# Kernel tuning notes

Hardware: AMD Instinct MI355X
Metric: run time of the kernel (lower is better)

## Reference

```python
import jax, jax.numpy as jnp
import numpy as np

CEP_ORDER = 24
ALPHA = 0.42
BETA = 0.2
ONSET = 2
IR_LENGTH = 128


def _freqt_matrix(in_order, out_order, alpha):
    # diffsptk FrequencyTransform precomputed matrix A (L2, L1): c2 = c1 @ A.T
    L1, L2 = in_order + 1, out_order + 1
    A = np.zeros((L2, L1), dtype=np.float64)
    A[0, :] = alpha ** np.arange(L1)
    if L2 > 1 and L1 > 1:
        A[1, 1:] = (alpha ** np.arange(L1 - 1, dtype=np.float64)) * np.arange(1, L1) * (1.0 - alpha * alpha)
    for i in range(2, L2):
        for j in range(1, L1):
            A[i, j] = A[i - 1, j - 1] + alpha * (A[i, j - 1] - A[i - 1, j])
    return A


def _mc2b_matrix(M, alpha):
    # b[m] = mc[m] - alpha*b[m+1]  =>  b[m] = sum_{j>=m} (-alpha)^(j-m) mc[j]
    j = np.arange(M + 1)
    P = j[None, :] - j[:, None]
    return np.where(P >= 0, (-alpha) ** np.maximum(P, 0), 0.0)


def _b2mc_matrix(M, alpha):
    # mc[m] = b[m] + alpha*b[m+1]
    return np.eye(M + 1) + alpha * np.eye(M + 1, k=1)


# constants derived from hyperparameters (buffers in the torch module)
A_FT = jnp.asarray(_freqt_matrix(CEP_ORDER, IR_LENGTH - 1, -ALPHA), dtype=jnp.float32)   # (128, 25)
A_MC2B = jnp.asarray(_mc2b_matrix(CEP_ORDER, ALPHA), dtype=jnp.float32)                  # (25, 25)
A_B2MC = jnp.asarray(_b2mc_matrix(CEP_ORDER, ALPHA), dtype=jnp.float32)                  # (25, 25)
_w = np.full(CEP_ORDER + 1, 1.0 + BETA, dtype=np.float32)
_w[:ONSET] = 1.0
WEIGHT = jnp.asarray(_w)                                                                  # (25,)


def _mc2en(mc):
    # mel-cepstrum -> energy: warp to linear cepstrum (len 128), power spectrum, r[0]
    c = jnp.einsum('...m,lm->...l', mc, A_FT)                 # (..., 128)
    spec = jnp.exp(2.0 * jnp.fft.rfft(c, n=IR_LENGTH).real)   # (..., 65), real power spectrum
    # r[0] of irfft(spec): DC + Nyquist once, interior bins twice (IR_LENGTH even)
    r0 = (spec[..., 0] + spec[..., -1] + 2.0 * jnp.sum(spec[..., 1:-1], axis=-1)) / IR_LENGTH
    return r0                                                  # (...,)


def setup_inputs() -> dict:
    key = jax.random.key(0)
    mc = 0.2 * jax.random.normal(key, (16, 32768, CEP_ORDER + 1), dtype=jnp.float32)
    return {"mc": mc}


def reference(mc):
    e1 = _mc2en(mc)                                            # energy before postfilter
    mc2 = mc * WEIGHT                                          # intensity-weighted cepstrum
    e2 = _mc2en(mc2)                                           # energy after weighting
    b2 = jnp.einsum('...m,nm->...n', mc2, A_MC2B)              # mc -> MLSA coefficients
    b2 = b2.at[..., 0].add(0.5 * jnp.log(e1 / e2))             # energy compensation on b[0]
    return jnp.einsum('...m,nm->...n', b2, A_B2MC)             # MLSA -> mel-cepstrum
```

## Files before the change

### kernel.cpp

```cpp
#include <hip/hip_runtime.h>


namespace cg {

constexpr int L  = 128;
constexpr int M1 = 25;

struct CosTab { double v[L]; };
constexpr CosTab make_costab() {
    CosTab t{};
    const double PI = 3.14159265358979323846;
    for (int i = 0; i < L; ++i) {
        int j = (i <= 64) ? i : i - 128;
        double x = (2.0 * PI * (double)j) / 128.0;
        double x2 = x * x, term = 1.0, s = 1.0;
        for (int n = 1; n <= 16; ++n) {
            term *= -x2 / ((2.0 * n - 1.0) * (2.0 * n));
            s += term;
        }
        t.v[i] = s;
    }
    return t;
}
constexpr CosTab CT = make_costab();

struct AMat { double v[L][M1]; };
constexpr AMat make_aft() {
    AMat A{};
    const double al = -0.42;
    double p = 1.0;
    for (int j = 0; j < M1; ++j) { A.v[0][j] = p; p *= al; }
    double q = 1.0;
    for (int j = 1; j < M1; ++j) { A.v[1][j] = q * (double)j * (1.0 - al * al); q *= al; }
    for (int i = 2; i < L; ++i)
        for (int j = 1; j < M1; ++j)
            A.v[i][j] = A.v[i - 1][j - 1] + al * (A.v[i][j - 1] - A.v[i - 1][j]);
    return A;
}
constexpr AMat AFT = make_aft();

struct Chunk { double v[8][M1]; };
template <int K0>
constexpr Chunk make_chunk() {
    Chunk c{};
    for (int kk = 0; kk < 8; ++kk) {
        int k = K0 + kk;
        for (int m = 0; m < M1; ++m) {
            double s = 0.0;
            for (int l = 0; l < L; ++l)
                s += AFT.v[l][m] * CT.v[(k * l) & 127];
            c.v[kk][m] = s;
        }
    }
    return c;
}
constexpr Chunk CH0 = make_chunk<0>();
constexpr Chunk CH1 = make_chunk<8>();
constexpr Chunk CH2 = make_chunk<16>();
constexpr Chunk CH3 = make_chunk<24>();
constexpr Chunk CH4 = make_chunk<32>();
constexpr Chunk CH5 = make_chunk<40>();
constexpr Chunk CH6 = make_chunk<48>();
constexpr Chunk CH7 = make_chunk<56>();
constexpr Chunk CH8 = make_chunk<64>();

constexpr double chunkval(int bin, int m) {
    const Chunk* chs[9] = { &CH0, &CH1, &CH2, &CH3, &CH4, &CH5, &CH6, &CH7, &CH8 };
    return chs[bin >> 3]->v[bin & 7][m];
}

constexpr double blogical(int k, int col) {
    const double LOG2E = 1.44269504088896340736;
    if (col >= 130) return (k == 25) ? -1.0e4 : 0.0;
    int bin = (col < 65) ? col : (col - 65);
    if (k == 25) return (bin == 0 || bin == 64) ? 0.0 : 1.0;
    if (k > 25) return 0.0;
    double c = LOG2E * 2.0 * chunkval(bin, k);
    if (col >= 65 && k >= 2) c *= 1.2;
    return c;
}

constexpr unsigned short f2h(double v) {
    if (v == 0.0) return 0;
    unsigned short s = 0;
    if (v < 0) { s = 0x8000; v = -v; }
    int e = 0;
    while (v >= 2.0) { v *= 0.5; ++e; }
    while (v < 1.0)  { v *= 2.0; --e; }
    if (e > 15) return (unsigned short)(s | 0x7c00);
    if (e < -14) return s;
    int mant = (int)((v - 1.0) * 1024.0 + 0.5);
    if (mant == 1024) { mant = 0; ++e; if (e > 15) return (unsigned short)(s | 0x7c00); }
    return (unsigned short)(s | ((e + 15) << 10) | mant);
}

struct Tile { unsigned short v[64][8]; };
template <int N>
constexpr Tile make_tile() {
    Tile t{};
    for (int l = 0; l < 64; ++l)
        for (int j = 0; j < 8; ++j)
            t.v[l][j] = f2h(blogical((l >> 4) * 8 + j, N * 16 + (l & 15)));
    return t;
}
constexpr Tile T0 = make_tile<0>();
constexpr Tile T1 = make_tile<1>();
constexpr Tile T2 = make_tile<2>();
constexpr Tile T3 = make_tile<3>();
constexpr Tile T4 = make_tile<4>();
constexpr Tile T5 = make_tile<5>();
constexpr Tile T6 = make_tile<6>();
constexpr Tile T7 = make_tile<7>();
constexpr Tile T8 = make_tile<8>();

struct BH { alignas(16) unsigned short v[9][64][8]; };
constexpr BH make_bh() {
    BH b{};
    const Tile* ts[9] = { &T0, &T1, &T2, &T3, &T4, &T5, &T6, &T7, &T8 };
    for (int n = 0; n < 9; ++n)
        for (int l = 0; l < 64; ++l)
            for (int j = 0; j < 8; ++j)
                b.v[n][l][j] = ts[n]->v[l][j];
    return b;
}

}

__device__ const cg::BH g_Bh = cg::make_bh();

typedef _Float16 f16x8 __attribute__((ext_vector_type(8)));
typedef float    f32x4 __attribute__((ext_vector_type(4)));

constexpr int WCHUNK = 1672;

__global__ __launch_bounds__(256, 6)
void mcpf_kernel(const float* __restrict__ mc, float* __restrict__ out) {
    __shared__ __align__(16) float sbuf[4 * WCHUNK];
    const int tid  = threadIdx.x;
    const int lane = tid & 63;
    const int wv   = tid >> 6;
    const int r0   = lane & 15;
    const int kg   = lane >> 4;

    float* __restrict__ wbuf = &sbuf[wv * WCHUNK];
    float* __restrict__ dreg = wbuf + 1600;

    const long long base4 = (long long)blockIdx.x * 1600 + wv * 400;

    f16x8 bfrag[9];
#pragma unroll
    for (int n = 0; n < 9; ++n)
        bfrag[n] = *reinterpret_cast<const f16x8*>(&g_Bh.v[n][lane][0]);

    const float4* __restrict__ src4 =
        reinterpret_cast<const float4*>(mc) + base4;
    float4* wb4 = reinterpret_cast<float4*>(wbuf);
#pragma unroll
    for (int j = 0; j < 7; ++j) {
        int idx = lane + j * 64;
        if (idx < 400) wb4[idx] = src4[idx];
    }
    asm volatile("s_waitcnt lgkmcnt(0)" ::: "memory");

#pragma unroll
    for (int g = 0; g < 4; ++g) {
        const int rowbase = g * 16;
        const float* __restrict__ arow = &wbuf[(rowbase + r0) * 25 + kg * 8];

        float tmp[8];
#pragma unroll
        for (int j = 0; j < 8; ++j) tmp[j] = arow[j];
        f16x8 af;
        af[0] = (_Float16)tmp[0];
        af[1] = (kg == 3) ? (_Float16)1.0f : (_Float16)tmp[1];
#pragma unroll
        for (int j = 2; j < 8; ++j)
            af[j] = (kg == 3) ? (_Float16)0.0f : (_Float16)tmp[j];

        float s1 = 0.0f, s2 = 0.0f;
#pragma unroll
        for (int n = 0; n < 9; ++n) {
            f32x4 acc = {0.f, 0.f, 0.f, 0.f};
            acc = __builtin_amdgcn_mfma_f32_16x16x32_f16(bfrag[n], af, acc, 0, 0, 0);
            float e0 = __builtin_amdgcn_exp2f(acc[0]);
            float e1 = __builtin_amdgcn_exp2f(acc[1]);
            float e2 = __builtin_amdgcn_exp2f(acc[2]);
            float e3 = __builtin_amdgcn_exp2f(acc[3]);
            if (n < 4) {
                s1 += (e0 + e1) + (e2 + e3);
            } else if (n == 4) {
                float h = (e0 + e1) + (e2 + e3);
                bool c = (kg == 0);
                s1 += c ? e0 : 0.0f;
                s2 += c ? (h - e0) : h;
            } else {
                s2 += (e0 + e1) + (e2 + e3);
            }
        }

        s1 += __shfl_xor(s1, 16);
        s1 += __shfl_xor(s1, 32);
        s2 += __shfl_xor(s2, 16);
        s2 += __shfl_xor(s2, 32);

        if (kg == 0) {
            float d = 0.34657359027997264f *
                      (__builtin_amdgcn_logf(s1) - __builtin_amdgcn_logf(s2));
            dreg[rowbase + r0] = d;
        }
    }

    asm volatile("s_waitcnt lgkmcnt(0)" ::: "memory");

    float4* __restrict__ dst4 = reinterpret_cast<float4*>(out) + base4;
#pragma unroll
    for (int j = 0; j < 7; ++j) {
        int idx = lane + j * 64;
        if (idx < 400) {
            float4 v = wb4[idx];
            int f = idx * 4;
            int q = f / 25;
            int r = f - 25 * q;
            float dv0 = dreg[q];
            float dv1 = dreg[q + 1];
            v.x *= (r     < 2)                  ? 1.0f : 1.2f;
            v.y *= (r + 1 < 2 || r + 1 == 25)   ? 1.0f : 1.2f;
            v.z *= (r + 2 == 25 || r + 2 == 26) ? 1.0f : 1.2f;
            v.w *= (r + 3 == 25 || r + 3 == 26) ? 1.0f : 1.2f;
            if (r == 0)  v.x += dv0;
            if (r == 22) v.w += dv1;
            if (r == 23) v.z += dv1;
            if (r == 24) v.y += dv1;
            dst4[idx] = v;
        }
    }
}

extern "C" void kernel_launch(void* const* d_in, const int* in_sizes, int n_in,
                              void* d_out, int out_size, void* d_ws, size_t ws_size,
                              hipStream_t stream) {
    const float* mc = (const float*)d_in[0];
    float* out = (float*)d_out;
    const int rows = in_sizes[0] / 25;
    const int blocks = rows / 256;
    mcpf_kernel<<<dim3(blocks), dim3(256), 0, stream>>>(mc, out);
}
```

Measured before the change: 24.54 us.

## Load rows directly from global into registers, dropping LDS staging

Removes the shared-memory staging buffer. Each lane now loads its 8-float slice of a row straight from global memory with unaligned 4-float vector loads and writes the scaled output back from registers, adding the energy correction inline. This cuts LDS traffic, the per-element div/mod index math and the waits, and lowers the occupancy hint from 6 to 4. Global accesses now use 100-byte row strides, so coalescing is worse, and loads issued as dword4 with only 4-byte alignment may be split.

After: 64.34 us. 162% more time.

```diff
diff --git a/kernel.cpp b/kernel.cpp
--- a/kernel.cpp
+++ b/kernel.cpp
@@ -130,52 +130,50 @@
 
 typedef _Float16 f16x8 __attribute__((ext_vector_type(8)));
 typedef float    f32x4 __attribute__((ext_vector_type(4)));
-
-constexpr int WCHUNK = 1672;
-
-__global__ __launch_bounds__(256, 6)
+typedef float    f32x4a4 __attribute__((ext_vector_type(4), aligned(4)));
+
+__global__ __launch_bounds__(256, 4)
 void mcpf_kernel(const float* __restrict__ mc, float* __restrict__ out) {
-    __shared__ __align__(16) float sbuf[4 * WCHUNK];
     const int tid  = threadIdx.x;
     const int lane = tid & 63;
     const int wv   = tid >> 6;
     const int r0   = lane & 15;
     const int kg   = lane >> 4;
 
-    float* __restrict__ wbuf = &sbuf[wv * WCHUNK];
-    float* __restrict__ dreg = wbuf + 1600;
-
-    const long long base4 = (long long)blockIdx.x * 1600 + wv * 400;
+    const long long row0 = (long long)blockIdx.x * 256 + wv * 64;
 
     f16x8 bfrag[9];
 #pragma unroll
     for (int n = 0; n < 9; ++n)
         bfrag[n] = *reinterpret_cast<const f16x8*>(&g_Bh.v[n][lane][0]);
 
-    const float4* __restrict__ src4 =
-        reinterpret_cast<const float4*>(mc) + base4;
-    float4* wb4 = reinterpret_cast<float4*>(wbuf);
-#pragma unroll
-    for (int j = 0; j < 7; ++j) {
-        int idx = lane + j * 64;
-        if (idx < 400) wb4[idx] = src4[idx];
-    }
-    asm volatile("s_waitcnt lgkmcnt(0)" ::: "memory");
-
+    f32x4a4 lv0[4], lv1[4];
+    float   f24[4];
 #pragma unroll
     for (int g = 0; g < 4; ++g) {
-        const int rowbase = g * 16;
-        const float* __restrict__ arow = &wbuf[(rowbase + r0) * 25 + kg * 8];
-
-        float tmp[8];
-#pragma unroll
-        for (int j = 0; j < 8; ++j) tmp[j] = arow[j];
+        const float* __restrict__ arow = mc + (row0 + g * 16 + r0) * 25;
+        if (kg < 3) {
+            lv0[g] = *reinterpret_cast<const f32x4a4*>(arow + kg * 8);
+            lv1[g] = *reinterpret_cast<const f32x4a4*>(arow + kg * 8 + 4);
+        } else {
+            f24[g] = arow[24];
+        }
+    }
+
+#pragma unroll
+    for (int g = 0; g < 4; ++g) {
         f16x8 af;
-        af[0] = (_Float16)tmp[0];
-        af[1] = (kg == 3) ? (_Float16)1.0f : (_Float16)tmp[1];
-#pragma unroll
-        for (int j = 2; j < 8; ++j)
-            af[j] = (kg == 3) ? (_Float16)0.0f : (_Float16)tmp[j];
+        if (kg < 3) {
+            af[0] = (_Float16)lv0[g].x; af[1] = (_Float16)lv0[g].y;
+            af[2] = (_Float16)lv0[g].z; af[3] = (_Float16)lv0[g].w;
+            af[4] = (_Float16)lv1[g].x; af[5] = (_Float16)lv1[g].y;
+            af[6] = (_Float16)lv1[g].z; af[7] = (_Float16)lv1[g].w;
+        } else {
+            af[0] = (_Float16)f24[g];
+            af[1] = (_Float16)1.0f;
+#pragma unroll
+            for (int j = 2; j < 8; ++j) af[j] = (_Float16)0.0f;
+        }
 
         float s1 = 0.0f, s2 = 0.0f;
 #pragma unroll
@@ -203,35 +201,29 @@
         s2 += __shfl_xor(s2, 16);
         s2 += __shfl_xor(s2, 32);
 
-        if (kg == 0) {
-            float d = 0.34657359027997264f *
-                      (__builtin_amdgcn_logf(s1) - __builtin_amdgcn_logf(s2));
-            dreg[rowbase + r0] = d;
-        }
-    }
-
-    asm volatile("s_waitcnt lgkmcnt(0)" ::: "memory");
-
-    float4* __restrict__ dst4 = reinterpret_cast<float4*>(out) + base4;
-#pragma unroll
-    for (int j = 0; j < 7; ++j) {
-        int idx = lane + j * 64;
-        if (idx < 400) {
-            float4 v = wb4[idx];
-            int f = idx * 4;
-            int q = f / 25;
-            int r = f - 25 * q;
-            float dv0 = dreg[q];
-            float dv1 = dreg[q + 1];
-            v.x *= (r     < 2)                  ? 1.0f : 1.2f;
-            v.y *= (r + 1 < 2 || r + 1 == 25)   ? 1.0f : 1.2f;
-            v.z *= (r + 2 == 25 || r + 2 == 26) ? 1.0f : 1.2f;
-            v.w *= (r + 3 == 25 || r + 3 == 26) ? 1.0f : 1.2f;
-            if (r == 0)  v.x += dv0;
-            if (r == 22) v.w += dv1;
-            if (r == 23) v.z += dv1;
-            if (r == 24) v.y += dv1;
-            dst4[idx] = v;
+        const float d = 0.34657359027997264f *
+                        (__builtin_amdgcn_logf(s1) - __builtin_amdgcn_logf(s2));
+
+        float* __restrict__ orow = out + (row0 + g * 16 + r0) * 25;
+        if (kg < 3) {
+            f32x4a4 o0, o1;
+            if (kg == 0) {
+                o0.x = lv0[g].x + d;
+                o0.y = lv0[g].y;
+            } else {
+                o0.x = 1.2f * lv0[g].x;
+                o0.y = 1.2f * lv0[g].y;
+            }
+            o0.z = 1.2f * lv0[g].z;
+            o0.w = 1.2f * lv0[g].w;
+            o1.x = 1.2f * lv1[g].x;
+            o1.y = 1.2f * lv1[g].y;
+            o1.z = 1.2f * lv1[g].z;
+            o1.w = 1.2f * lv1[g].w;
+            *reinterpret_cast<f32x4a4*>(orow + kg * 8)     = o0;
+            *reinterpret_cast<f32x4a4*>(orow + kg * 8 + 4) = o1;
+        } else {
+            orow[24] = 1.2f * f24[g];
         }
     }
 }
```

## Load input directly into LDS and fuse per-group output writeback via shuffles

Applied to the files above, without the earlier changes.

Input rows are now staged with global_load_lds straight into shared memory instead of passing through registers, and the wait changes from lgkmcnt to vmcnt. The separate writeback pass, which used an LDS scratch area for per-row energy corrections, is folded into each 16-row MFMA group. Each group's correction is taken from the computing lanes with a cross-lane shuffle, so the scratch region and its extra LDS round trip are gone. This interleaves stores with compute and trims LDS use, at the cost of more divergent store code and shuffles inside the group loop.

Measured after the change: 24.69 us. Within noise of the previous version (+0.6%).

```diff
diff --git a/kernel.cpp b/kernel.cpp
--- a/kernel.cpp
+++ b/kernel.cpp
@@ -131,20 +131,16 @@
 typedef _Float16 f16x8 __attribute__((ext_vector_type(8)));
 typedef float    f32x4 __attribute__((ext_vector_type(4)));
 
-constexpr int WCHUNK = 1672;
-
 __global__ __launch_bounds__(256, 6)
 void mcpf_kernel(const float* __restrict__ mc, float* __restrict__ out) {
-    __shared__ __align__(16) float sbuf[4 * WCHUNK];
+    __shared__ __align__(16) float sbuf[4 * 1600 + 16];
     const int tid  = threadIdx.x;
     const int lane = tid & 63;
     const int wv   = tid >> 6;
     const int r0   = lane & 15;
     const int kg   = lane >> 4;
 
-    float* __restrict__ wbuf = &sbuf[wv * WCHUNK];
-    float* __restrict__ dreg = wbuf + 1600;
-
+    float* __restrict__ wbuf = &sbuf[wv * 1600];
     const long long base4 = (long long)blockIdx.x * 1600 + wv * 400;
 
     f16x8 bfrag[9];
@@ -154,18 +150,24 @@
 
     const float4* __restrict__ src4 =
         reinterpret_cast<const float4*>(mc) + base4;
-    float4* wb4 = reinterpret_cast<float4*>(wbuf);
 #pragma unroll
     for (int j = 0; j < 7; ++j) {
         int idx = lane + j * 64;
-        if (idx < 400) wb4[idx] = src4[idx];
-    }
-    asm volatile("s_waitcnt lgkmcnt(0)" ::: "memory");
+        if (idx < 400) {
+            __builtin_amdgcn_global_load_lds(
+                (const __attribute__((address_space(1))) float*)(const float*)(src4 + idx),
+                (__attribute__((address_space(3))) float*)(wbuf + j * 256),
+                16, 0, 0);
+        }
+    }
+    asm volatile("s_waitcnt vmcnt(0)" ::: "memory");
+
+    float4* __restrict__ wb4  = reinterpret_cast<float4*>(wbuf);
+    float4* __restrict__ dst4 = reinterpret_cast<float4*>(out) + base4;
 
 #pragma unroll
     for (int g = 0; g < 4; ++g) {
-        const int rowbase = g * 16;
-        const float* __restrict__ arow = &wbuf[(rowbase + r0) * 25 + kg * 8];
+        const float* __restrict__ arow = &wbuf[(g * 16 + r0) * 25 + kg * 8];
 
         float tmp[8];
 #pragma unroll
@@ -203,35 +205,30 @@
         s2 += __shfl_xor(s2, 16);
         s2 += __shfl_xor(s2, 32);
 
-        if (kg == 0) {
-            float d = 0.34657359027997264f *
-                      (__builtin_amdgcn_logf(s1) - __builtin_amdgcn_logf(s2));
-            dreg[rowbase + r0] = d;
-        }
-    }
-
-    asm volatile("s_waitcnt lgkmcnt(0)" ::: "memory");
-
-    float4* __restrict__ dst4 = reinterpret_cast<float4*>(out) + base4;
-#pragma unroll
-    for (int j = 0; j < 7; ++j) {
-        int idx = lane + j * 64;
-        if (idx < 400) {
-            float4 v = wb4[idx];
-            int f = idx * 4;
-            int q = f / 25;
-            int r = f - 25 * q;
-            float dv0 = dreg[q];
-            float dv1 = dreg[q + 1];
-            v.x *= (r     < 2)                  ? 1.0f : 1.2f;
-            v.y *= (r + 1 < 2 || r + 1 == 25)   ? 1.0f : 1.2f;
-            v.z *= (r + 2 == 25 || r + 2 == 26) ? 1.0f : 1.2f;
-            v.w *= (r + 3 == 25 || r + 3 == 26) ? 1.0f : 1.2f;
-            if (r == 0)  v.x += dv0;
-            if (r == 22) v.w += dv1;
-            if (r == 23) v.z += dv1;
-            if (r == 24) v.y += dv1;
-            dst4[idx] = v;
+        const float d = 0.34657359027997264f *
+                        (__builtin_amdgcn_logf(s1) - __builtin_amdgcn_logf(s2));
+
+#pragma unroll
+        for (int j = 0; j < 2; ++j) {
+            int t = lane + j * 64;
+            if (t < 100) {
+                int idx = g * 100 + t;
+                float4 v = wb4[idx];
+                int f = idx * 4;
+                int q = f / 25;
+                int r = f - 25 * q;
+                int srcl = ((r == 0) ? q : q + 1) & 15;
+                float dv = __shfl(d, srcl);
+                v.x *= (r     < 2)                  ? 1.0f : 1.2f;
+                v.y *= (r + 1 < 2 || r + 1 == 25)   ? 1.0f : 1.2f;
+                v.z *= (r + 2 == 25 || r + 2 == 26) ? 1.0f : 1.2f;
+                v.w *= (r + 3 == 25 || r + 3 == 26) ? 1.0f : 1.2f;
+                if (r == 0)  v.x += dv;
+                if (r == 22) v.w += dv;
+                if (r == 23) v.z += dv;
+                if (r == 24) v.y += dv;
+                dst4[idx] = v;
+            }
         }
     }
 }
```
